# Kernel optimization log

Measured on AMD Instinct MI355X. Metric: run time of the kernel, lower is better.

Reference implementation:

```python
import jax, jax.numpy as jnp
import numpy as np

G, IN_D, OUT_D, KQ_D = 8192, 512, 512, 128
EPS = 1e-12  # torch F.normalize default eps


def setup_inputs() -> dict:
    key = jax.random.key(0)
    ks = jax.random.split(key, 7)
    s_in = 1.0 / np.sqrt(IN_D)
    return {
        "x": jax.random.normal(ks[0], (G, IN_D), dtype=jnp.float32),
        "Wk": jax.random.uniform(ks[1], (KQ_D, IN_D), jnp.float32, -s_in, s_in),
        "bk": jax.random.uniform(ks[2], (KQ_D,), jnp.float32, -s_in, s_in),
        "Wq": jax.random.uniform(ks[3], (KQ_D, IN_D), jnp.float32, -s_in, s_in),
        "bq": jax.random.uniform(ks[4], (KQ_D,), jnp.float32, -s_in, s_in),
        "Wv": jax.random.uniform(ks[5], (OUT_D, IN_D), jnp.float32, -s_in, s_in),
        "bv": jax.random.uniform(ks[6], (OUT_D,), jnp.float32, -s_in, s_in),
    }


def reference(x, Wk, bk, Wq, bq, Wv, bv):
    # QKV projections (torch Linear: x @ W^T + b)
    k = x @ Wk.T + bk            # [g, kq]
    q = x @ Wq.T + bq            # [g, kq]
    v = x @ Wv.T + bv            # [g, outD]
    # g x g attention scores
    scores = k @ q.T             # [g, g]
    # L2-normalize each row (F.normalize with dim=-1): x / max(||x||_2, eps)
    norm = jnp.sqrt(jnp.sum(scores * scores, axis=-1, keepdims=True))
    scores_n = scores / jnp.maximum(norm, EPS)
    # value matmul + residual
    return scores_n @ v + v      # [g, outD]
```

## Files before the change

### kernel.cpp

```cpp
#include <hip/hip_runtime.h>
#include <hip/hip_bf16.h>
#include <stdint.h>

typedef __attribute__((ext_vector_type(8))) short bf16x8;
typedef __attribute__((ext_vector_type(4))) float f32x4;

__device__ __forceinline__ unsigned short f2bf(float f) {
  union { float f; uint32_t u; } v; v.f = f;
  uint32_t u = v.u;
  return (unsigned short)((u + 0x7fffu + ((u >> 16) & 1u)) >> 16);
}
__device__ __forceinline__ float bf2f(unsigned short h) {
  union { uint32_t u; float f; } v; v.u = ((uint32_t)h) << 16;
  return v.f;
}

#define GLL(g, l) __builtin_amdgcn_global_load_lds( \
    (const __attribute__((address_space(1))) void*)(g), \
    (__attribute__((address_space(3))) void*)(l), 16, 0, 0)

__global__ void cvt_all(const float* __restrict__ x,
                        const float* __restrict__ wk, const float* __restrict__ wq,
                        const float* __restrict__ wv,
                        unsigned short* __restrict__ xb, unsigned short* __restrict__ wb) {
  const int i = (blockIdx.x * 256 + threadIdx.x) * 4;
  const float* src; unsigned short* dst; int off;
  if (i < 4194304) { src = x; dst = xb; off = i; }
  else {
    const int j = i - 4194304;
    dst = wb; 
    if (j < 65536)       { src = wk; off = j; }
    else if (j < 131072) { src = wq; off = j - 65536; }
    else                 { src = wv; off = j - 131072; }
    dst = wb + (j - off);
  }
  const float4 v = *(const float4*)(src + off);
  ushort4 o; o.x = f2bf(v.x); o.y = f2bf(v.y); o.z = f2bf(v.z); o.w = f2bf(v.w);
  *(ushort4*)(dst + off) = o;
}

__global__ __launch_bounds__(256) void qkv_gemm(
    const unsigned short* __restrict__ xb, const unsigned short* __restrict__ wb,
    const float* __restrict__ pbk, const float* __restrict__ pbq, const float* __restrict__ pbv,
    unsigned short* __restrict__ kb, unsigned short* __restrict__ qtb,
    unsigned short* __restrict__ vb, unsigned short* __restrict__ vtb)
{
  __shared__ unsigned short Alds[2][128 * 64];
  __shared__ unsigned short Blds[2][128 * 64];
  const int tid = threadIdx.x;
  const int lane = tid & 63;
  const int wid = tid >> 6;
  const int wm = wid >> 1, wn = wid & 1;
  const int m0 = blockIdx.x * 128, n0 = blockIdx.y * 128;
  const int l15 = lane & 15, l4 = lane >> 4;

  f32x4 acc[4][4] = {};

  auto stage = [&](int b, int kt) {
    const int k0 = kt * 64;
    #pragma unroll
    for (int p = 0; p < 4; ++p) {
      const int e = p * 256 + tid;
      const int row = e >> 3;
      const int cs = (e & 7) ^ (row & 7);
      GLL(xb + (size_t)(m0 + row) * 512 + k0 + cs * 8, &Alds[b][(p * 256 + (tid & ~63)) * 8]);
      GLL(wb + (size_t)(n0 + row) * 512 + k0 + cs * 8, &Blds[b][(p * 256 + (tid & ~63)) * 8]);
    }
  };

  stage(0, 0);
  __syncthreads();

  for (int kt = 0; kt < 8; ++kt) {
    const int cur = kt & 1;
    if (kt < 7) stage(cur ^ 1, kt + 1);
    #pragma unroll
    for (int kk = 0; kk < 2; ++kk) {
      bf16x8 af[4], bfv[4];
      #pragma unroll
      for (int i = 0; i < 4; ++i) {
        const int ra = wm * 64 + i * 16 + l15;
        const int c  = kk * 4 + l4;
        af[i]  = *(const bf16x8*)(&Alds[cur][ra * 64 + ((c ^ (ra & 7)) * 8)]);
        const int rb = wn * 64 + i * 16 + l15;
        bfv[i] = *(const bf16x8*)(&Blds[cur][rb * 64 + ((c ^ (rb & 7)) * 8)]);
      }
      #pragma unroll
      for (int i = 0; i < 4; ++i)
        #pragma unroll
        for (int j = 0; j < 4; ++j)
          acc[i][j] = __builtin_amdgcn_mfma_f32_16x16x32_bf16(af[i], bfv[j], acc[i][j], 0, 0, 0);
    }
    __syncthreads();
  }

  #pragma unroll
  for (int i = 0; i < 4; ++i) {
    #pragma unroll
    for (int j = 0; j < 4; ++j) {
      const int rbase = m0 + wm * 64 + i * 16 + l4 * 4;
      const int c = n0 + wn * 64 + j * 16 + l15;
      const float bias = (c < 128) ? pbk[c] : (c < 256) ? pbq[c - 128] : pbv[c - 256];
      unsigned short o[4];
      #pragma unroll
      for (int r = 0; r < 4; ++r) o[r] = f2bf(acc[i][j][r] + bias);
      if (c < 128) {
        #pragma unroll
        for (int r = 0; r < 4; ++r) kb[(size_t)(rbase + r) * 128 + c] = o[r];
      } else if (c < 256) {
        ushort4 t; t.x = o[0]; t.y = o[1]; t.z = o[2]; t.w = o[3];
        *(ushort4*)(qtb + (size_t)(c - 128) * 8192 + rbase) = t;
      } else {
        #pragma unroll
        for (int r = 0; r < 4; ++r) vb[(size_t)(rbase + r) * 512 + (c - 256)] = o[r];
        ushort4 t; t.x = o[0]; t.y = o[1]; t.z = o[2]; t.w = o[3];
        *(ushort4*)(vtb + (size_t)(c - 256) * 8192 + rbase) = t;
      }
    }
  }
}

__global__ __launch_bounds__(512) void gh_gemm(
    const unsigned short* __restrict__ qtb, const unsigned short* __restrict__ vtb,
    unsigned short* __restrict__ pb)
{
  __shared__ unsigned short Alds[2][128 * 64];
  __shared__ unsigned short Blds[2][80 * 64];
  const int tid = threadIdx.x, lane = tid & 63, wid = tid >> 6;
  const int l15 = lane & 15, l4 = lane >> 4;
  const int kc = blockIdx.x, nq = blockIdx.y;
  const int g0 = kc * 256;
  const int m0 = wid * 16;

  f32x4 acc[5] = {};

  auto stage = [&](int b, int st) {
    const int gs = g0 + st * 64;
    #pragma unroll
    for (int p = 0; p < 2; ++p) {
      const int e = p * 512 + tid;
      const int row = e >> 3;
      const int cs = (e & 7) ^ (row & 7);
      GLL(qtb + (size_t)row * 8192 + gs + cs * 8, &Alds[b][(p * 512 + (tid & ~63)) * 8]);
    }
    {
      const int row = tid >> 3;
      const int cglob = nq * 80 + row;
      const unsigned short* src = (cglob < 128) ? (qtb + (size_t)cglob * 8192)
                                                : (vtb + (size_t)(cglob - 128) * 8192);
      const int cs = (tid & 7) ^ (row & 7);
      GLL(src + gs + cs * 8, &Blds[b][(tid & ~63) * 8]);
    }
    if (tid < 128) {
      const int e = 512 + tid;
      const int row = e >> 3;
      const int cglob = nq * 80 + row;
      const unsigned short* src = (cglob < 128) ? (qtb + (size_t)cglob * 8192)
                                                : (vtb + (size_t)(cglob - 128) * 8192);
      const int cs = (e & 7) ^ (row & 7);
      GLL(src + gs + cs * 8, &Blds[b][(512 + (tid & ~63)) * 8]);
    }
  };

  stage(0, 0);
  __syncthreads();

  for (int st = 0; st < 4; ++st) {
    const int cur = st & 1;
    if (st < 3) stage(cur ^ 1, st + 1);
    #pragma unroll
    for (int ks = 0; ks < 2; ++ks) {
      const int ra = m0 + l15;
      const int ca = ks * 4 + l4;
      const bf16x8 af = *(const bf16x8*)(&Alds[cur][ra * 64 + ((ca ^ (ra & 7)) * 8)]);
      #pragma unroll
      for (int nf = 0; nf < 5; ++nf) {
        const int rb = nf * 16 + l15;
        const bf16x8 bf = *(const bf16x8*)(&Blds[cur][rb * 64 + ((ca ^ (rb & 7)) * 8)]);
        acc[nf] = __builtin_amdgcn_mfma_f32_16x16x32_bf16(af, bf, acc[nf], 0, 0, 0);
      }
    }
    __syncthreads();
  }

  #pragma unroll
  for (int nf = 0; nf < 5; ++nf) {
    const int col = nq * 80 + nf * 16 + l15;
    #pragma unroll
    for (int r = 0; r < 4; ++r) {
      const int row = m0 + l4 * 4 + r;
      pb[((size_t)kc * 128 + row) * 640 + col] = f2bf(acc[nf][r]);
    }
  }
}

__global__ void gh_finalize(const unsigned short* __restrict__ pb,
                            unsigned short* __restrict__ Gb, unsigned short* __restrict__ Hbt) {
  const int idx = blockIdx.x * 256 + threadIdx.x;
  float s = 0.f;
  #pragma unroll
  for (int p = 0; p < 32; ++p) s += bf2f(pb[(size_t)p * 81920 + idx]);
  const int m = idx / 640, c = idx % 640;
  if (c < 128) Gb[m * 128 + c] = f2bf(s);
  else         Hbt[(size_t)(c - 128) * 128 + m] = f2bf(s);
}

__global__ __launch_bounds__(512) void tnorm_uv(
    const unsigned short* __restrict__ kb, const unsigned short* __restrict__ Gb,
    const unsigned short* __restrict__ Hbt, const unsigned short* __restrict__ vb,
    float* __restrict__ out)
{
  __shared__ float ssq_part[4][32];
  __shared__ float rnorm_lds[32];
  const int tid = threadIdx.x, lane = tid & 63, wid = tid >> 6;
  const int l15 = lane & 15, l4 = lane >> 4;
  const int m0 = blockIdx.x * 32;
  const int mf = wid & 1, nq = wid >> 1;
  const int rowbase = m0 + mf * 16;

  bf16x8 af[4];
  #pragma unroll
  for (int ks = 0; ks < 4; ++ks)
    af[ks] = *(const bf16x8*)(kb + (size_t)(rowbase + l15) * 128 + ks * 32 + l4 * 8);

  f32x4 tac[2] = {};
  #pragma unroll
  for (int ks = 0; ks < 4; ++ks) {
    #pragma unroll
    for (int t = 0; t < 2; ++t) {
      const int nf = nq * 2 + t;
      const bf16x8 bf = *(const bf16x8*)(Gb + (size_t)(nf * 16 + l15) * 128 + ks * 32 + l4 * 8);
      tac[t] = __builtin_amdgcn_mfma_f32_16x16x32_bf16(af[ks], bf, tac[t], 0, 0, 0);
    }
  }
  float ssq[4] = {0.f, 0.f, 0.f, 0.f};
  #pragma unroll
  for (int t = 0; t < 2; ++t) {
    const int col = (nq * 2 + t) * 16 + l15;
    #pragma unroll
    for (int r = 0; r < 4; ++r) {
      const int row = rowbase + l4 * 4 + r;
      ssq[r] += tac[t][r] * bf2f(kb[(size_t)row * 128 + col]);
    }
  }
  #pragma unroll
  for (int d = 1; d < 16; d <<= 1)
    #pragma unroll
    for (int r = 0; r < 4; ++r) ssq[r] += __shfl_xor(ssq[r], d);
  if (l15 == 0) {
    #pragma unroll
    for (int r = 0; r < 4; ++r) ssq_part[nq][mf * 16 + l4 * 4 + r] = ssq[r];
  }
  __syncthreads();
  if (tid < 32) {
    const float s = ssq_part[0][tid] + ssq_part[1][tid] + ssq_part[2][tid] + ssq_part[3][tid];
    rnorm_lds[tid] = 1.0f / fmaxf(sqrtf(s), 1e-12f);
  }
  __syncthreads();

  f32x4 acc[8] = {};
  #pragma unroll
  for (int ks = 0; ks < 4; ++ks) {
    #pragma unroll
    for (int nf = 0; nf < 8; ++nf) {
      const int col = nq * 128 + nf * 16 + l15;
      const bf16x8 bf = *(const bf16x8*)(Hbt + (size_t)col * 128 + ks * 32 + l4 * 8);
      acc[nf] = __builtin_amdgcn_mfma_f32_16x16x32_bf16(af[ks], bf, acc[nf], 0, 0, 0);
    }
  }

  float rn[4];
  #pragma unroll
  for (int r = 0; r < 4; ++r) rn[r] = rnorm_lds[mf * 16 + l4 * 4 + r];

  #pragma unroll
  for (int nf = 0; nf < 8; ++nf) {
    const int col = nq * 128 + nf * 16 + l15;
    #pragma unroll
    for (int r = 0; r < 4; ++r) {
      const int row = rowbase + l4 * 4 + r;
      out[(size_t)row * 512 + col] =
          acc[nf][r] * rn[r] + bf2f(vb[(size_t)row * 512 + col]);
    }
  }
}

extern "C" void kernel_launch(void* const* d_in, const int* in_sizes, int n_in,
                              void* d_out, int out_size, void* d_ws, size_t ws_size,
                              hipStream_t stream) {
  const float* x  = (const float*)d_in[0];
  const float* Wk = (const float*)d_in[1];
  const float* bk = (const float*)d_in[2];
  const float* Wq = (const float*)d_in[3];
  const float* bq = (const float*)d_in[4];
  const float* Wv = (const float*)d_in[5];
  const float* bv = (const float*)d_in[6];
  float* out = (float*)d_out;

  char* ws = (char*)d_ws;
  unsigned short* xb   = (unsigned short*)(ws);
  unsigned short* wb   = (unsigned short*)(ws + 8388608);
  unsigned short* kb   = (unsigned short*)(ws + 9175040);
  unsigned short* vb   = (unsigned short*)(ws + 11272192);
  unsigned short* vtb  = (unsigned short*)(ws + 19660800);
  unsigned short* qtb  = (unsigned short*)(ws + 28049408);
  unsigned short* pb   = (unsigned short*)(ws + 30146560);
  unsigned short* Gb   = (unsigned short*)(ws + 35389440);
  unsigned short* Hbt  = (unsigned short*)(ws + 35422208);

  cvt_all<<<4480, 256, 0, stream>>>(x, Wk, Wq, Wv, xb, wb);
  qkv_gemm<<<dim3(64, 6), 256, 0, stream>>>(xb, wb, bk, bq, bv, kb, qtb, vb, vtb);
  gh_gemm<<<dim3(32, 8), 512, 0, stream>>>(qtb, vtb, pb);
  gh_finalize<<<320, 256, 0, stream>>>(pb, Gb, Hbt);
  tnorm_uv<<<256, 512, 0, stream>>>(kb, Gb, Hbt, vb, out);
}
```

Measured before the change: 53.23 us.

## Halve qkv_gemm and tnorm_uv tile heights to launch more workgroups

qkv_gemm now uses 64x128 tiles on a 1D grid of 768 workgroups, with a remapped block index that spreads tiles across XCDs. It also sets launch_bounds to 3 blocks per CU. tnorm_uv now handles 16 rows per block with 8 waves splitting the columns, which doubles the grid to 512 blocks. The aim is to fill the 256 CUs better on the small problem, at the cost of more redundant B-tile loads and less reuse per tile.

Result: no change. 52.37 us (-1.6%).

```diff
diff --git a/kernel.cpp b/kernel.cpp
--- a/kernel.cpp
+++ b/kernel.cpp
@@ -28,7 +28,6 @@
   if (i < 4194304) { src = x; dst = xb; off = i; }
   else {
     const int j = i - 4194304;
-    dst = wb; 
     if (j < 65536)       { src = wk; off = j; }
     else if (j < 131072) { src = wq; off = j - 65536; }
     else                 { src = wv; off = j - 131072; }
@@ -39,31 +38,40 @@
   *(ushort4*)(dst + off) = o;
 }
 
-__global__ __launch_bounds__(256) void qkv_gemm(
+__global__ __launch_bounds__(256, 3) void qkv_gemm(
     const unsigned short* __restrict__ xb, const unsigned short* __restrict__ wb,
     const float* __restrict__ pbk, const float* __restrict__ pbq, const float* __restrict__ pbv,
     unsigned short* __restrict__ kb, unsigned short* __restrict__ qtb,
     unsigned short* __restrict__ vb, unsigned short* __restrict__ vtb)
 {
-  __shared__ unsigned short Alds[2][128 * 64];
+  __shared__ unsigned short Alds[2][64 * 64];
   __shared__ unsigned short Blds[2][128 * 64];
   const int tid = threadIdx.x;
   const int lane = tid & 63;
   const int wid = tid >> 6;
   const int wm = wid >> 1, wn = wid & 1;
-  const int m0 = blockIdx.x * 128, n0 = blockIdx.y * 128;
+  const int wg = blockIdx.x;
+  const int s = (wg & 7) * 96 + (wg >> 3);
+  const int bx = s & 127, by = s >> 7;
+  const int m0 = bx * 64, n0 = by * 128;
   const int l15 = lane & 15, l4 = lane >> 4;
 
-  f32x4 acc[4][4] = {};
+  f32x4 acc[2][4] = {};
 
   auto stage = [&](int b, int kt) {
     const int k0 = kt * 64;
+    #pragma unroll
+    for (int p = 0; p < 2; ++p) {
+      const int e = p * 256 + tid;
+      const int row = e >> 3;
+      const int cs = (e & 7) ^ (row & 7);
+      GLL(xb + (size_t)(m0 + row) * 512 + k0 + cs * 8, &Alds[b][(p * 256 + (tid & ~63)) * 8]);
+    }
     #pragma unroll
     for (int p = 0; p < 4; ++p) {
       const int e = p * 256 + tid;
       const int row = e >> 3;
       const int cs = (e & 7) ^ (row & 7);
-      GLL(xb + (size_t)(m0 + row) * 512 + k0 + cs * 8, &Alds[b][(p * 256 + (tid & ~63)) * 8]);
       GLL(wb + (size_t)(n0 + row) * 512 + k0 + cs * 8, &Blds[b][(p * 256 + (tid & ~63)) * 8]);
     }
   };
@@ -76,17 +84,21 @@
     if (kt < 7) stage(cur ^ 1, kt + 1);
     #pragma unroll
     for (int kk = 0; kk < 2; ++kk) {
-      bf16x8 af[4], bfv[4];
-      #pragma unroll
-      for (int i = 0; i < 4; ++i) {
-        const int ra = wm * 64 + i * 16 + l15;
+      bf16x8 af[2], bfv[4];
+      #pragma unroll
+      for (int i = 0; i < 2; ++i) {
+        const int ra = wm * 32 + i * 16 + l15;
         const int c  = kk * 4 + l4;
-        af[i]  = *(const bf16x8*)(&Alds[cur][ra * 64 + ((c ^ (ra & 7)) * 8)]);
-        const int rb = wn * 64 + i * 16 + l15;
-        bfv[i] = *(const bf16x8*)(&Blds[cur][rb * 64 + ((c ^ (rb & 7)) * 8)]);
+        af[i] = *(const bf16x8*)(&Alds[cur][ra * 64 + ((c ^ (ra & 7)) * 8)]);
       }
       #pragma unroll
-      for (int i = 0; i < 4; ++i)
+      for (int j = 0; j < 4; ++j) {
+        const int rb = wn * 64 + j * 16 + l15;
+        const int c  = kk * 4 + l4;
+        bfv[j] = *(const bf16x8*)(&Blds[cur][rb * 64 + ((c ^ (rb & 7)) * 8)]);
+      }
+      #pragma unroll
+      for (int i = 0; i < 2; ++i)
         #pragma unroll
         for (int j = 0; j < 4; ++j)
           acc[i][j] = __builtin_amdgcn_mfma_f32_16x16x32_bf16(af[i], bfv[j], acc[i][j], 0, 0, 0);
@@ -95,10 +107,10 @@
   }
 
   #pragma unroll
-  for (int i = 0; i < 4; ++i) {
+  for (int i = 0; i < 2; ++i) {
     #pragma unroll
     for (int j = 0; j < 4; ++j) {
-      const int rbase = m0 + wm * 64 + i * 16 + l4 * 4;
+      const int rbase = m0 + wm * 32 + i * 16 + l4 * 4;
       const int c = n0 + wn * 64 + j * 16 + l15;
       const float bias = (c < 128) ? pbk[c] : (c < 256) ? pbq[c - 128] : pbv[c - 256];
       unsigned short o[4];
@@ -210,38 +222,28 @@
     const unsigned short* __restrict__ Hbt, const unsigned short* __restrict__ vb,
     float* __restrict__ out)
 {
-  __shared__ float ssq_part[4][32];
-  __shared__ float rnorm_lds[32];
+  __shared__ float ssq_part[8][16];
+  __shared__ float rnorm_lds[16];
   const int tid = threadIdx.x, lane = tid & 63, wid = tid >> 6;
   const int l15 = lane & 15, l4 = lane >> 4;
-  const int m0 = blockIdx.x * 32;
-  const int mf = wid & 1, nq = wid >> 1;
-  const int rowbase = m0 + mf * 16;
+  const int rowbase = blockIdx.x * 16;
 
   bf16x8 af[4];
   #pragma unroll
   for (int ks = 0; ks < 4; ++ks)
     af[ks] = *(const bf16x8*)(kb + (size_t)(rowbase + l15) * 128 + ks * 32 + l4 * 8);
 
-  f32x4 tac[2] = {};
+  f32x4 tac = {};
   #pragma unroll
   for (int ks = 0; ks < 4; ++ks) {
-    #pragma unroll
-    for (int t = 0; t < 2; ++t) {
-      const int nf = nq * 2 + t;
-      const bf16x8 bf = *(const bf16x8*)(Gb + (size_t)(nf * 16 + l15) * 128 + ks * 32 + l4 * 8);
-      tac[t] = __builtin_amdgcn_mfma_f32_16x16x32_bf16(af[ks], bf, tac[t], 0, 0, 0);
-    }
-  }
-  float ssq[4] = {0.f, 0.f, 0.f, 0.f};
-  #pragma unroll
-  for (int t = 0; t < 2; ++t) {
-    const int col = (nq * 2 + t) * 16 + l15;
-    #pragma unroll
-    for (int r = 0; r < 4; ++r) {
-      const int row = rowbase + l4 * 4 + r;
-      ssq[r] += tac[t][r] * bf2f(kb[(size_t)row * 128 + col]);
-    }
+    const bf16x8 bf = *(const bf16x8*)(Gb + (size_t)(wid * 16 + l15) * 128 + ks * 32 + l4 * 8);
+    tac = __builtin_amdgcn_mfma_f32_16x16x32_bf16(af[ks], bf, tac, 0, 0, 0);
+  }
+  float ssq[4];
+  #pragma unroll
+  for (int r = 0; r < 4; ++r) {
+    const int row = rowbase + l4 * 4 + r;
+    ssq[r] = tac[r] * bf2f(kb[(size_t)row * 128 + wid * 16 + l15]);
   }
   #pragma unroll
   for (int d = 1; d < 16; d <<= 1)
@@ -249,21 +251,23 @@
     for (int r = 0; r < 4; ++r) ssq[r] += __shfl_xor(ssq[r], d);
   if (l15 == 0) {
     #pragma unroll
-    for (int r = 0; r < 4; ++r) ssq_part[nq][mf * 16 + l4 * 4 + r] = ssq[r];
+    for (int r = 0; r < 4; ++r) ssq_part[wid][l4 * 4 + r] = ssq[r];
   }
   __syncthreads();
-  if (tid < 32) {
-    const float s = ssq_part[0][tid] + ssq_part[1][tid] + ssq_part[2][tid] + ssq_part[3][tid];
+  if (tid < 16) {
+    float s = 0.f;
+    #pragma unroll
+    for (int w = 0; w < 8; ++w) s += ssq_part[w][tid];
     rnorm_lds[tid] = 1.0f / fmaxf(sqrtf(s), 1e-12f);
   }
   __syncthreads();
 
-  f32x4 acc[8] = {};
+  f32x4 acc[4] = {};
   #pragma unroll
   for (int ks = 0; ks < 4; ++ks) {
     #pragma unroll
-    for (int nf = 0; nf < 8; ++nf) {
-      const int col = nq * 128 + nf * 16 + l15;
+    for (int nf = 0; nf < 4; ++nf) {
+      const int col = wid * 64 + nf * 16 + l15;
       const bf16x8 bf = *(const bf16x8*)(Hbt + (size_t)col * 128 + ks * 32 + l4 * 8);
       acc[nf] = __builtin_amdgcn_mfma_f32_16x16x32_bf16(af[ks], bf, acc[nf], 0, 0, 0);
     }
@@ -271,11 +275,11 @@
 
   float rn[4];
   #pragma unroll
-  for (int r = 0; r < 4; ++r) rn[r] = rnorm_lds[mf * 16 + l4 * 4 + r];
-
-  #pragma unroll
-  for (int nf = 0; nf < 8; ++nf) {
-    const int col = nq * 128 + nf * 16 + l15;
+  for (int r = 0; r < 4; ++r) rn[r] = rnorm_lds[l4 * 4 + r];
+
+  #pragma unroll
+  for (int nf = 0; nf < 4; ++nf) {
+    const int col = wid * 64 + nf * 16 + l15;
     #pragma unroll
     for (int r = 0; r < 4; ++r) {
       const int row = rowbase + l4 * 4 + r;
@@ -309,8 +313,8 @@
   unsigned short* Hbt  = (unsigned short*)(ws + 35422208);
 
   cvt_all<<<4480, 256, 0, stream>>>(x, Wk, Wq, Wv, xb, wb);
-  qkv_gemm<<<dim3(64, 6), 256, 0, stream>>>(xb, wb, bk, bq, bv, kb, qtb, vb, vtb);
+  qkv_gemm<<<768, 256, 0, stream>>>(xb, wb, bk, bq, bv, kb, qtb, vb, vtb);
   gh_gemm<<<dim3(32, 8), 512, 0, stream>>>(qtb, vtb, pb);
   gh_finalize<<<320, 256, 0, stream>>>(pb, Gb, Hbt);
-  tnorm_uv<<<256, 512, 0, stream>>>(kb, Gb, Hbt, vb, out);
-}
+  tnorm_uv<<<512, 512, 0, stream>>>(kb, Gb, Hbt, vb, out);
+}
```
